# Performance work log

Hardware: AMD Instinct MI355X
Metric: run time of the kernel (lower is better)

The kernel has to match this reference:

```python
import jax, jax.numpy as jnp
import numpy as np

H = 256          # hidden_channels
NP, NJ, NC = 8192, 8192, 4096  # person / job_posting / company node counts
EA, EW, EP = 262144, 131072, 131072  # edge counts per relation


def _gcn(x_src, W, b, edge_index, num_src, num_dst):
    """Bipartite GCNConv: h = x_src @ W; out[dst] = sum_e norm_e * h[src_e] + b,
    norm = deg_out(src)^-1/2 * deg_in(dst)^-1/2 (symmetric GCN normalization)."""
    h = x_src @ W                                # [num_src, H]
    row, col = edge_index[0], edge_index[1]
    ones = jnp.ones(row.shape[0], dtype=h.dtype)
    deg_src = jax.ops.segment_sum(ones, row, num_segments=num_src)
    deg_dst = jax.ops.segment_sum(ones, col, num_segments=num_dst)
    dis_src = jnp.where(deg_src > 0, jax.lax.rsqrt(jnp.maximum(deg_src, 1e-12)), 0.0)
    dis_dst = jnp.where(deg_dst > 0, jax.lax.rsqrt(jnp.maximum(deg_dst, 1e-12)), 0.0)
    norm = dis_src[row] * dis_dst[col]           # [E]
    out = jax.ops.segment_sum(h[row] * norm[:, None], col, num_segments=num_dst)
    return out + b


def setup_inputs() -> dict:
    key = jax.random.key(0)
    ks = jax.random.split(key, 12)
    s = 1.0 / np.sqrt(H)
    return {
        "x_person":  jax.random.normal(ks[0], (NP, H), jnp.float32),
        "x_job":     jax.random.normal(ks[1], (NJ, H), jnp.float32),
        "x_company": jax.random.normal(ks[2], (NC, H), jnp.float32),
        "ei_applied": jax.random.randint(ks[3], (2, EA), 0, 8192, jnp.int64 if jax.config.read('jax_enable_x64') else jnp.int32),
        "ei_worked":  jax.random.randint(ks[4], (2, EW), 0, 4096, jnp.int64 if jax.config.read('jax_enable_x64') else jnp.int32),
        "ei_posted":  jax.random.randint(ks[5], (2, EP), 0, 4096, jnp.int64 if jax.config.read('jax_enable_x64') else jnp.int32),
        "W_aj": jax.random.normal(ks[6], (H, H), jnp.float32) * s,
        "b_aj": jnp.zeros((H,), jnp.float32),
        "W_wa": jax.random.normal(ks[7], (H, H), jnp.float32) * s,
        "b_wa": jnp.zeros((H,), jnp.float32),
        "W_pb": jax.random.normal(ks[8], (H, H), jnp.float32) * s,
        "b_pb": jnp.zeros((H,), jnp.float32),
    }


def reference(x_person, x_job, x_company, ei_applied, ei_worked, ei_posted,
              W_aj, b_aj, W_wa, b_wa, W_pb, b_pb):
    Np, Nj, Nc = x_person.shape[0], x_job.shape[0], x_company.shape[0]
    # HeteroConv with aggr='sum': each dst type sums messages over its edge types
    job_emb = _gcn(x_person, W_aj, b_aj, ei_applied, Np, Nj)
    comp_emb = (_gcn(x_person, W_wa, b_wa, ei_worked, Np, Nc)
                + _gcn(x_job, W_pb, b_pb, ei_posted, Nj, Nc))  # computed but unused downstream
    del comp_emb
    person_emb = x_person  # 'person' is never a dst type; features pass through
    scores = jax.nn.sigmoid(person_emb @ job_emb.T)  # [Np, Nj]
    return scores
```

## Files before the change

kernel.cpp:

```cpp
#include <hip/hip_runtime.h>
#include <hip/hip_bf16.h>

#define HCH 256
#define NPN 8192
#define NJN 8192
#define EAE 262144
#define CAP 96

typedef _Float16 f16x8 __attribute__((ext_vector_type(8)));
typedef _Float16 f16x4 __attribute__((ext_vector_type(4)));
typedef float f32x4 __attribute__((ext_vector_type(4)));

typedef __attribute__((address_space(1))) void glb_void;
typedef __attribute__((address_space(3))) void lds_void;

#define WS_CUR   0
#define WS_DEG   32768
#define WS_CSR2  65536
#define WS_XH    3211264
#define WS_ZH    7405568
#define WS_GH    11599872
#define WS_WHT   15794176

__global__ void k_init(int* __restrict__ cnt, const float* __restrict__ W,
                       _Float16* __restrict__ WhT, const float* __restrict__ x,
                       _Float16* __restrict__ Xh) {
    int bid = blockIdx.x, t = threadIdx.x;
    if (bid < 64) {
        cnt[bid * 256 + t] = 0;
    } else if (bid < 320) {
        int idx = (bid - 64) * 256 + t;
        int n = idx >> 8, k = idx & 255;
        WhT[idx] = (_Float16)W[k * HCH + n];
    } else {
        int i = ((bid - 320) * 256 + t) * 4;
        float4 v = *(const float4*)(x + i);
        f16x4 h;
        h[0] = (_Float16)v.x; h[1] = (_Float16)v.y;
        h[2] = (_Float16)v.z; h[3] = (_Float16)v.w;
        *(f16x4*)(Xh + i) = h;
    }
}

__global__ void k_edge(const int* __restrict__ row, const int* __restrict__ col,
                       int* __restrict__ deg_src, int* __restrict__ cur,
                       int* __restrict__ csr2) {
    int e = blockIdx.x * 256 + threadIdx.x;
    int r = row[e], c = col[e];
    atomicAdd(&deg_src[r], 1);
    int p = atomicAdd(&cur[c], 1);
    if (p < CAP) csr2[c * CAP + p] = r;
}

__global__ __launch_bounds__(64)
void k_agg(const _Float16* __restrict__ Xh, const int* __restrict__ csr2,
           const int* __restrict__ cur, const int* __restrict__ deg_src,
           _Float16* __restrict__ Zh) {
    int j = blockIdx.x;
    int t = threadIdx.x;
    int degt = cur[j];
    int deg = degt > CAP ? CAP : degt;

    __shared__ int   sidx[CAP];
    __shared__ float sw[CAP];
    for (int b = t; b < deg; b += 64) {
        int s = csr2[j * CAP + b];
        sidx[b] = s;
        sw[b] = rsqrtf((float)deg_src[s]);
    }
    __syncthreads();

    float a0 = 0.f, a1 = 0.f, a2 = 0.f, a3 = 0.f;
    const _Float16* xb = Xh + t * 4;
    int e = 0;
    for (; e + 4 <= deg; e += 4) {
        int s0 = sidx[e], s1 = sidx[e + 1], s2 = sidx[e + 2], s3 = sidx[e + 3];
        float w0 = sw[e], w1 = sw[e + 1], w2 = sw[e + 2], w3 = sw[e + 3];
        f16x4 v0 = *(const f16x4*)(xb + (size_t)s0 * HCH);
        f16x4 v1 = *(const f16x4*)(xb + (size_t)s1 * HCH);
        f16x4 v2 = *(const f16x4*)(xb + (size_t)s2 * HCH);
        f16x4 v3 = *(const f16x4*)(xb + (size_t)s3 * HCH);
        a0 += w0 * (float)v0[0] + w1 * (float)v1[0] + w2 * (float)v2[0] + w3 * (float)v3[0];
        a1 += w0 * (float)v0[1] + w1 * (float)v1[1] + w2 * (float)v2[1] + w3 * (float)v3[1];
        a2 += w0 * (float)v0[2] + w1 * (float)v1[2] + w2 * (float)v2[2] + w3 * (float)v3[2];
        a3 += w0 * (float)v0[3] + w1 * (float)v1[3] + w2 * (float)v2[3] + w3 * (float)v3[3];
    }
    for (; e < deg; e++) {
        int s0 = sidx[e];
        float w0 = sw[e];
        f16x4 v0 = *(const f16x4*)(xb + (size_t)s0 * HCH);
        a0 += w0 * (float)v0[0]; a1 += w0 * (float)v0[1];
        a2 += w0 * (float)v0[2]; a3 += w0 * (float)v0[3];
    }
    f16x4 out;
    if (degt > 0) {
        float dd = rsqrtf((float)degt);
        out[0] = (_Float16)(a0 * dd); out[1] = (_Float16)(a1 * dd);
        out[2] = (_Float16)(a2 * dd); out[3] = (_Float16)(a3 * dd);
    } else {
        out[0] = out[1] = out[2] = out[3] = (_Float16)0.f;
    }
    *(f16x4*)(Zh + (size_t)j * HCH + t * 4) = out;
}

template <int TM, int TN>
__global__ __launch_bounds__(256, 2)
void k_gemm(const _Float16* __restrict__ A, const _Float16* __restrict__ Bt,
            const float* __restrict__ bias, _Float16* __restrict__ Cout, int Ncols) {
    constexpr int WM = TM / 2, WN = TN / 2;
    constexpr int MR = WM / 16, NR = WN / 16;
    constexpr int CHA = TM * 8 / 256;
    constexpr int CHB = TN * 8 / 256;
    constexpr int BOFF = TM * 128;

    __shared__ _Float16 sm[2][(TM + TN) * 64];

    int tid = threadIdx.x;
    int wid = tid >> 6, lane = tid & 63;

    int brow = blockIdx.y * TM;
    int bcol = blockIdx.x * TN;
    int wrow = (wid >> 1) * WM;
    int wcol = (wid & 1) * WN;

    f32x4 acc[MR][NR] = {};

    int lr = lane & 15;
    int kq = lane >> 4;

    auto stage = [&](int t, int b) {
        int k0 = t * 64;
#pragma unroll
        for (int i = 0; i < CHA; i++) {
            int wc0 = i * 256 + wid * 64;
            int c = wc0 + lane;
            int r = c >> 3, cc = c & 7;
            const char* ga = (const char*)A +
                (size_t)(brow + r) * (HCH * 2) + (size_t)(k0 + cc * 8) * 2;
            __builtin_amdgcn_global_load_lds(
                (glb_void*)ga, (lds_void*)((char*)sm[b] + wc0 * 16), 16, 0, 0);
        }
#pragma unroll
        for (int i = 0; i < CHB; i++) {
            int wc0 = i * 256 + wid * 64;
            int c = wc0 + lane;
            int r = c >> 3, cc = c & 7;
            const char* gb = (const char*)Bt +
                (size_t)(bcol + r) * (HCH * 2) + (size_t)(k0 + cc * 8) * 2;
            __builtin_amdgcn_global_load_lds(
                (glb_void*)gb, (lds_void*)((char*)sm[b] + BOFF + wc0 * 16), 16, 0, 0);
        }
    };

    stage(0, 0);
    __syncthreads();

    constexpr int NT = HCH / 64;
#pragma unroll
    for (int t = 0; t < NT; t++) {
        int cur = t & 1;
        if (t + 1 < NT) stage(t + 1, cur ^ 1);
        const char* base = (const char*)sm[cur];
#pragma unroll
        for (int kk = 0; kk < 64; kk += 32) {
            f16x8 af[MR], bfr[NR];
            int kbyte = (kk + kq * 8) * 2;
#pragma unroll
            for (int m = 0; m < MR; m++) {
                int r = wrow + m * 16 + lr;
                af[m] = *(const f16x8*)(base + r * 128 + kbyte);
            }
#pragma unroll
            for (int n = 0; n < NR; n++) {
                int r = wcol + n * 16 + lr;
                bfr[n] = *(const f16x8*)(base + BOFF + r * 128 + kbyte);
            }
#pragma unroll
            for (int m = 0; m < MR; m++)
#pragma unroll
                for (int n = 0; n < NR; n++)
                    acc[m][n] = __builtin_amdgcn_mfma_f32_16x16x32_f16(
                        af[m], bfr[n], acc[m][n], 0, 0, 0);
        }
        __syncthreads();
    }

    int rq = lane >> 4;
#pragma unroll
    for (int m = 0; m < MR; m++) {
#pragma unroll
        for (int n = 0; n < NR; n++) {
#pragma unroll
            for (int j = 0; j < 4; j++) {
                int gr = brow + wrow + m * 16 + rq * 4 + j;
                int gc = bcol + wcol + n * 16 + lr;
                float v = acc[m][n][j] + bias[gc];
                Cout[(size_t)gr * Ncols + gc] = (_Float16)v;
            }
        }
    }
}

#define G2_NW 32
__global__ __launch_bounds__(512, 1)
void k_gemm2(const _Float16* __restrict__ A, const _Float16* __restrict__ Bt,
             float* __restrict__ C) {
    __shared__ _Float16 smA[128 * HCH];
    __shared__ _Float16 smB[2][64 * HCH];
    __shared__ float    smC[128 * 64];

    int tid = threadIdx.x;
    int wid = tid >> 6, lane = tid & 63;
    int lr = lane & 15, kq = lane >> 4;

    int id = blockIdx.x;
    int xcd = id & 7, slot = id >> 3;
    int cg = xcd >> 1;
    int strip = slot + (xcd & 1) * 32;
    int brow = strip * 128;
    int bcol0 = cg * (64 * G2_NW);

    int wrow = (wid >> 1) * 32;
    int wcol = (wid & 1) * 32;

#pragma unroll
    for (int i = 0; i < 8; i++) {
        int wc0 = i * 512 + wid * 64;
        int c = wc0 + lane;
        int r = c >> 5, q = c & 31;
        int j = q ^ (r & 7);
        const char* ga = (const char*)(A + (size_t)(brow + r) * HCH + j * 8);
        __builtin_amdgcn_global_load_lds(
            (glb_void*)ga, (lds_void*)((char*)smA + wc0 * 16), 16, 0, 0);
    }
    auto stageB = [&](int t, int b) {
#pragma unroll
        for (int i = 0; i < 4; i++) {
            int wc0 = i * 512 + wid * 64;
            int c = wc0 + lane;
            int r = c >> 5, q = c & 31;
            int j = q ^ (r & 7);
            const char* gb = (const char*)(Bt +
                (size_t)(bcol0 + t * 64 + r) * HCH + j * 8);
            __builtin_amdgcn_global_load_lds(
                (glb_void*)gb, (lds_void*)((char*)smB[b] + wc0 * 16), 16, 0, 0);
        }
    };
    stageB(0, 0);
    __syncthreads();

    const char* sA = (const char*)smA;
    f16x8 areg[2][8];
#pragma unroll
    for (int m = 0; m < 2; m++) {
#pragma unroll
        for (int ks = 0; ks < 8; ks++) {
            int r = wrow + m * 16 + lr;
            int sb = ks * 4 + kq;
            areg[m][ks] = *(const f16x8*)(sA + r * 512 + ((sb ^ (r & 7)) << 4));
        }
    }

    for (int t = 0; t < G2_NW; t++) {
        int cb = t & 1;
        if (t + 1 < G2_NW) stageB(t + 1, cb ^ 1);
        __builtin_amdgcn_sched_barrier(0);
        const char* sB = (const char*)smB[cb];
        f32x4 acc[2][2] = {};
        __builtin_amdgcn_s_setprio(1);
#pragma unroll
        for (int ks = 0; ks < 8; ks++) {
            f16x8 bf2[2];
            int sb = ks * 4 + kq;
#pragma unroll
            for (int n = 0; n < 2; n++) {
                int r = wcol + n * 16 + lr;
                bf2[n] = *(const f16x8*)(sB + r * 512 + ((sb ^ (r & 7)) << 4));
            }
#pragma unroll
            for (int m = 0; m < 2; m++)
#pragma unroll
                for (int n = 0; n < 2; n++)
                    acc[m][n] = __builtin_amdgcn_mfma_f32_16x16x32_f16(
                        bf2[n], areg[m][ks], acc[m][n], 0, 0, 0);
        }
        __builtin_amdgcn_s_setprio(0);

#pragma unroll
        for (int m = 0; m < 2; m++) {
#pragma unroll
            for (int n = 0; n < 2; n++) {
                int row = wrow + m * 16 + lr;
                int ch = ((wcol + n * 16) >> 2) + kq;
                int sc = ch ^ (row & 7);
                *(f32x4*)(smC + row * 64 + sc * 4) = acc[m][n];
            }
        }

        int bcol = bcol0 + t * 64;
        int ch = (wcol >> 2) + (lane & 7);
#pragma unroll
        for (int p = 0; p < 4; p++) {
            int row = wrow + p * 8 + (lane >> 3);
            int sc = ch ^ (row & 7);
            f32x4 v = *(const f32x4*)(smC + row * 64 + sc * 4);
            f32x4 o;
#pragma unroll
            for (int j = 0; j < 4; j++) {
                float e = __expf(-v[j]);
                o[j] = __builtin_amdgcn_rcpf(1.f + e);
            }
            __builtin_nontemporal_store(
                o, (f32x4*)(C + (size_t)(brow + row) * NJN + bcol + ch * 4));
        }

        if (t + 1 < G2_NW) {
            __builtin_amdgcn_sched_barrier(0);
            asm volatile("s_waitcnt vmcnt(4)" ::: "memory");
            __builtin_amdgcn_s_barrier();
            __builtin_amdgcn_sched_barrier(0);
        }
    }
}

extern "C" void kernel_launch(void* const* d_in, const int* in_sizes, int n_in,
                              void* d_out, int out_size, void* d_ws, size_t ws_size,
                              hipStream_t stream) {
    const float* x_person = (const float*)d_in[0];
    const int*   ei_app   = (const int*)d_in[3];
    const float* W_aj     = (const float*)d_in[6];
    const float* b_aj     = (const float*)d_in[7];

    const int* erow = ei_app;
    const int* ecol = ei_app + EAE;

    char* w = (char*)d_ws;
    int*      cur     = (int*)(w + WS_CUR);
    int*      deg_src = (int*)(w + WS_DEG);
    int*      csr2    = (int*)(w + WS_CSR2);
    _Float16* Xh      = (_Float16*)(w + WS_XH);
    _Float16* Zh      = (_Float16*)(w + WS_ZH);
    _Float16* Gh      = (_Float16*)(w + WS_GH);
    _Float16* WhT     = (_Float16*)(w + WS_WHT);

    k_init<<<2368, 256, 0, stream>>>(cur, W_aj, WhT, x_person, Xh);
    k_edge<<<EAE / 256, 256, 0, stream>>>(erow, ecol, deg_src, cur, csr2);
    k_agg<<<NJN, 64, 0, stream>>>(Xh, csr2, cur, deg_src, Zh);
    {
        dim3 grid(HCH / 128, NJN / 64);
        k_gemm<64, 128><<<grid, 256, 0, stream>>>(Zh, WhT, b_aj, Gh, HCH);
    }
    k_gemm2<<<256, 512, 0, stream>>>(Xh, Gh, (float*)d_out);
}
```

Before: 126.2 us.

## Fuse neighbor aggregation with the W projection GEMM into one kernel

Replaces the separate aggregation kernel and the small GEMM with one kernel. Each 512-thread block aggregates 32 job rows into swizzled LDS and then multiplies them by W, streaming W tiles through double-buffered LDS, before writing Gh. This removes the Zh round trip through global memory and one launch. In exchange there are only 256 blocks of 512 threads at one block per CU, so the gather phase may have less latency hiding than the old 8192 small blocks.

```diff
diff --git a/kernel.cpp b/kernel.cpp
--- a/kernel.cpp
+++ b/kernel.cpp
@@ -18,7 +18,6 @@
 #define WS_DEG   32768
 #define WS_CSR2  65536
 #define WS_XH    3211264
-#define WS_ZH    7405568
 #define WS_GH    11599872
 #define WS_WHT   15794176
 
@@ -52,151 +51,121 @@
     if (p < CAP) csr2[c * CAP + p] = r;
 }
 
-__global__ __launch_bounds__(64)
-void k_agg(const _Float16* __restrict__ Xh, const int* __restrict__ csr2,
-           const int* __restrict__ cur, const int* __restrict__ deg_src,
-           _Float16* __restrict__ Zh) {
-    int j = blockIdx.x;
-    int t = threadIdx.x;
-    int degt = cur[j];
-    int deg = degt > CAP ? CAP : degt;
-
-    __shared__ int   sidx[CAP];
-    __shared__ float sw[CAP];
-    for (int b = t; b < deg; b += 64) {
-        int s = csr2[j * CAP + b];
-        sidx[b] = s;
-        sw[b] = rsqrtf((float)deg_src[s]);
-    }
-    __syncthreads();
-
-    float a0 = 0.f, a1 = 0.f, a2 = 0.f, a3 = 0.f;
-    const _Float16* xb = Xh + t * 4;
-    int e = 0;
-    for (; e + 4 <= deg; e += 4) {
-        int s0 = sidx[e], s1 = sidx[e + 1], s2 = sidx[e + 2], s3 = sidx[e + 3];
-        float w0 = sw[e], w1 = sw[e + 1], w2 = sw[e + 2], w3 = sw[e + 3];
-        f16x4 v0 = *(const f16x4*)(xb + (size_t)s0 * HCH);
-        f16x4 v1 = *(const f16x4*)(xb + (size_t)s1 * HCH);
-        f16x4 v2 = *(const f16x4*)(xb + (size_t)s2 * HCH);
-        f16x4 v3 = *(const f16x4*)(xb + (size_t)s3 * HCH);
-        a0 += w0 * (float)v0[0] + w1 * (float)v1[0] + w2 * (float)v2[0] + w3 * (float)v3[0];
-        a1 += w0 * (float)v0[1] + w1 * (float)v1[1] + w2 * (float)v2[1] + w3 * (float)v3[1];
-        a2 += w0 * (float)v0[2] + w1 * (float)v1[2] + w2 * (float)v2[2] + w3 * (float)v3[2];
-        a3 += w0 * (float)v0[3] + w1 * (float)v1[3] + w2 * (float)v2[3] + w3 * (float)v3[3];
-    }
-    for (; e < deg; e++) {
-        int s0 = sidx[e];
-        float w0 = sw[e];
-        f16x4 v0 = *(const f16x4*)(xb + (size_t)s0 * HCH);
-        a0 += w0 * (float)v0[0]; a1 += w0 * (float)v0[1];
-        a2 += w0 * (float)v0[2]; a3 += w0 * (float)v0[3];
-    }
-    f16x4 out;
-    if (degt > 0) {
-        float dd = rsqrtf((float)degt);
-        out[0] = (_Float16)(a0 * dd); out[1] = (_Float16)(a1 * dd);
-        out[2] = (_Float16)(a2 * dd); out[3] = (_Float16)(a3 * dd);
-    } else {
-        out[0] = out[1] = out[2] = out[3] = (_Float16)0.f;
-    }
-    *(f16x4*)(Zh + (size_t)j * HCH + t * 4) = out;
-}
-
-template <int TM, int TN>
-__global__ __launch_bounds__(256, 2)
-void k_gemm(const _Float16* __restrict__ A, const _Float16* __restrict__ Bt,
-            const float* __restrict__ bias, _Float16* __restrict__ Cout, int Ncols) {
-    constexpr int WM = TM / 2, WN = TN / 2;
-    constexpr int MR = WM / 16, NR = WN / 16;
-    constexpr int CHA = TM * 8 / 256;
-    constexpr int CHB = TN * 8 / 256;
-    constexpr int BOFF = TM * 128;
-
-    __shared__ _Float16 sm[2][(TM + TN) * 64];
+__global__ __launch_bounds__(512, 1)
+void k_aggemm1(const _Float16* __restrict__ Xh, const int* __restrict__ csr2,
+               const int* __restrict__ cur, const int* __restrict__ deg_src,
+               const _Float16* __restrict__ WhT, const float* __restrict__ bias,
+               _Float16* __restrict__ Gh) {
+    __shared__ _Float16 smZ[32 * HCH];
+    __shared__ _Float16 smW[2][64 * HCH];
+    __shared__ int      sidxAll[8][96];
+    __shared__ float    swAll[8][96];
 
     int tid = threadIdx.x;
     int wid = tid >> 6, lane = tid & 63;
-
-    int brow = blockIdx.y * TM;
-    int bcol = blockIdx.x * TN;
-    int wrow = (wid >> 1) * WM;
-    int wcol = (wid & 1) * WN;
-
-    f32x4 acc[MR][NR] = {};
-
-    int lr = lane & 15;
-    int kq = lane >> 4;
-
-    auto stage = [&](int t, int b) {
-        int k0 = t * 64;
-#pragma unroll
-        for (int i = 0; i < CHA; i++) {
-            int wc0 = i * 256 + wid * 64;
+    int lr = lane & 15, kq = lane >> 4;
+    int brow = blockIdx.x * 32;
+
+    auto stageB = [&](int ct, int b) {
+#pragma unroll
+        for (int i = 0; i < 4; i++) {
+            int wc0 = i * 512 + wid * 64;
             int c = wc0 + lane;
-            int r = c >> 3, cc = c & 7;
-            const char* ga = (const char*)A +
-                (size_t)(brow + r) * (HCH * 2) + (size_t)(k0 + cc * 8) * 2;
+            int r = c >> 5, q = c & 31;
+            int j = q ^ (r & 7);
+            const char* gb = (const char*)(WhT +
+                (size_t)(ct * 64 + r) * HCH + j * 8);
             __builtin_amdgcn_global_load_lds(
-                (glb_void*)ga, (lds_void*)((char*)sm[b] + wc0 * 16), 16, 0, 0);
-        }
-#pragma unroll
-        for (int i = 0; i < CHB; i++) {
-            int wc0 = i * 256 + wid * 64;
-            int c = wc0 + lane;
-            int r = c >> 3, cc = c & 7;
-            const char* gb = (const char*)Bt +
-                (size_t)(bcol + r) * (HCH * 2) + (size_t)(k0 + cc * 8) * 2;
-            __builtin_amdgcn_global_load_lds(
-                (glb_void*)gb, (lds_void*)((char*)sm[b] + BOFF + wc0 * 16), 16, 0, 0);
+                (glb_void*)gb, (lds_void*)((char*)smW[b] + wc0 * 16), 16, 0, 0);
         }
     };
-
-    stage(0, 0);
+    stageB(0, 0);
+
+    int* sidx = sidxAll[wid];
+    float* sw = swAll[wid];
+#pragma unroll
+    for (int pass = 0; pass < 4; pass++) {
+        int jloc = pass * 8 + wid;
+        int j = brow + jloc;
+        int degt = cur[j];
+        int deg = degt > CAP ? CAP : degt;
+        for (int b = lane; b < deg; b += 64) {
+            int s = csr2[j * CAP + b];
+            sidx[b] = s;
+            sw[b] = rsqrtf((float)deg_src[s]);
+        }
+        float a0 = 0.f, a1 = 0.f, a2 = 0.f, a3 = 0.f;
+        const _Float16* xb = Xh + lane * 4;
+        int e = 0;
+        for (; e + 4 <= deg; e += 4) {
+            int s0 = sidx[e], s1 = sidx[e + 1], s2 = sidx[e + 2], s3 = sidx[e + 3];
+            float w0 = sw[e], w1 = sw[e + 1], w2 = sw[e + 2], w3 = sw[e + 3];
+            f16x4 v0 = *(const f16x4*)(xb + (size_t)s0 * HCH);
+            f16x4 v1 = *(const f16x4*)(xb + (size_t)s1 * HCH);
+            f16x4 v2 = *(const f16x4*)(xb + (size_t)s2 * HCH);
+            f16x4 v3 = *(const f16x4*)(xb + (size_t)s3 * HCH);
+            a0 += w0 * (float)v0[0] + w1 * (float)v1[0] + w2 * (float)v2[0] + w3 * (float)v3[0];
+            a1 += w0 * (float)v0[1] + w1 * (float)v1[1] + w2 * (float)v2[1] + w3 * (float)v3[1];
+            a2 += w0 * (float)v0[2] + w1 * (float)v1[2] + w2 * (float)v2[2] + w3 * (float)v3[2];
+            a3 += w0 * (float)v0[3] + w1 * (float)v1[3] + w2 * (float)v2[3] + w3 * (float)v3[3];
+        }
+        for (; e < deg; e++) {
+            int s0 = sidx[e];
+            float w0 = sw[e];
+            f16x4 v0 = *(const f16x4*)(xb + (size_t)s0 * HCH);
+            a0 += w0 * (float)v0[0]; a1 += w0 * (float)v0[1];
+            a2 += w0 * (float)v0[2]; a3 += w0 * (float)v0[3];
+        }
+        f16x4 out;
+        if (degt > 0) {
+            float dd = rsqrtf((float)degt);
+            out[0] = (_Float16)(a0 * dd); out[1] = (_Float16)(a1 * dd);
+            out[2] = (_Float16)(a2 * dd); out[3] = (_Float16)(a3 * dd);
+        } else {
+            out[0] = out[1] = out[2] = out[3] = (_Float16)0.f;
+        }
+        int byteoff = jloc * 512 + (((lane >> 1) ^ (jloc & 7)) << 4) + (lane & 1) * 8;
+        *(f16x4*)((char*)smZ + byteoff) = out;
+    }
     __syncthreads();
 
-    constexpr int NT = HCH / 64;
-#pragma unroll
-    for (int t = 0; t < NT; t++) {
-        int cur = t & 1;
-        if (t + 1 < NT) stage(t + 1, cur ^ 1);
-        const char* base = (const char*)sm[cur];
-#pragma unroll
-        for (int kk = 0; kk < 64; kk += 32) {
-            f16x8 af[MR], bfr[NR];
-            int kbyte = (kk + kq * 8) * 2;
-#pragma unroll
-            for (int m = 0; m < MR; m++) {
-                int r = wrow + m * 16 + lr;
-                af[m] = *(const f16x8*)(base + r * 128 + kbyte);
-            }
-#pragma unroll
-            for (int n = 0; n < NR; n++) {
-                int r = wcol + n * 16 + lr;
-                bfr[n] = *(const f16x8*)(base + BOFF + r * 128 + kbyte);
-            }
-#pragma unroll
-            for (int m = 0; m < MR; m++)
-#pragma unroll
-                for (int n = 0; n < NR; n++)
-                    acc[m][n] = __builtin_amdgcn_mfma_f32_16x16x32_f16(
-                        af[m], bfr[n], acc[m][n], 0, 0, 0);
-        }
-        __syncthreads();
-    }
-
-    int rq = lane >> 4;
-#pragma unroll
-    for (int m = 0; m < MR; m++) {
-#pragma unroll
-        for (int n = 0; n < NR; n++) {
-#pragma unroll
-            for (int j = 0; j < 4; j++) {
-                int gr = brow + wrow + m * 16 + rq * 4 + j;
-                int gc = bcol + wcol + n * 16 + lr;
-                float v = acc[m][n][j] + bias[gc];
-                Cout[(size_t)gr * Ncols + gc] = (_Float16)v;
-            }
+    int m = wid >> 2, n = wid & 3;
+    int arow = m * 16 + lr;
+
+    f16x8 areg[8];
+#pragma unroll
+    for (int ks = 0; ks < 8; ks++) {
+        int sb = ks * 4 + kq;
+        areg[ks] = *(const f16x8*)((const char*)smZ + arow * 512 +
+                                   ((sb ^ (arow & 7)) << 4));
+    }
+
+    for (int ct = 0; ct < 4; ct++) {
+        int cb = ct & 1;
+        if (ct + 1 < 4) stageB(ct + 1, cb ^ 1);
+        __builtin_amdgcn_sched_barrier(0);
+        const char* sB = (const char*)smW[cb];
+        f32x4 acc = {};
+#pragma unroll
+        for (int ks = 0; ks < 8; ks++) {
+            int sb = ks * 4 + kq;
+            int r = n * 16 + lr;
+            f16x8 bf = *(const f16x8*)(sB + r * 512 + ((sb ^ (r & 7)) << 4));
+            acc = __builtin_amdgcn_mfma_f32_16x16x32_f16(bf, areg[ks], acc, 0, 0, 0);
+        }
+        int gr = brow + m * 16 + lr;
+        int gc0 = ct * 64 + n * 16 + kq * 4;
+        float4 bv = *(const float4*)(bias + gc0);
+        f16x4 o;
+        o[0] = (_Float16)(acc[0] + bv.x); o[1] = (_Float16)(acc[1] + bv.y);
+        o[2] = (_Float16)(acc[2] + bv.z); o[3] = (_Float16)(acc[3] + bv.w);
+        *(f16x4*)(Gh + (size_t)gr * HCH + gc0) = o;
+
+        if (ct + 1 < 4) {
+            __builtin_amdgcn_sched_barrier(0);
+            asm volatile("s_waitcnt vmcnt(1)" ::: "memory");
+            __builtin_amdgcn_s_barrier();
+            __builtin_amdgcn_sched_barrier(0);
         }
     }
 }
@@ -215,10 +184,10 @@
 
     int id = blockIdx.x;
     int xcd = id & 7, slot = id >> 3;
-    int cg = xcd >> 1;
+    int cg2 = xcd >> 1;
     int strip = slot + (xcd & 1) * 32;
     int brow = strip * 128;
-    int bcol0 = cg * (64 * G2_NW);
+    int bcol0 = cg2 * (64 * G2_NW);
 
     int wrow = (wid >> 1) * 32;
     int wcol = (wid & 1) * 32;
@@ -339,16 +308,12 @@
     int*      deg_src = (int*)(w + WS_DEG);
     int*      csr2    = (int*)(w + WS_CSR2);
     _Float16* Xh      = (_Float16*)(w + WS_XH);
-    _Float16* Zh      = (_Float16*)(w + WS_ZH);
     _Float16* Gh      = (_Float16*)(w + WS_GH);
     _Float16* WhT     = (_Float16*)(w + WS_WHT);
 
     k_init<<<2368, 256, 0, stream>>>(cur, W_aj, WhT, x_person, Xh);
     k_edge<<<EAE / 256, 256, 0, stream>>>(erow, ecol, deg_src, cur, csr2);
-    k_agg<<<NJN, 64, 0, stream>>>(Xh, csr2, cur, deg_src, Zh);
-    {
-        dim3 grid(HCH / 128, NJN / 64);
-        k_gemm<64, 128><<<grid, 256, 0, stream>>>(Zh, WhT, b_aj, Gh, HCH);
-    }
+    k_aggemm1<<<NJN / 32, 512, 0, stream>>>(Xh, csr2, cur, deg_src, WhT,
+                                            b_aj, Gh);
     k_gemm2<<<256, 512, 0, stream>>>(Xh, Gh, (float*)d_out);
 }
```

After: 133.0 us. +5.3%, slower.

## Load B tiles directly from global into registers, dropping LDS double buffer

Applied to the files above, without the earlier changes.

The final sigmoid GEMM no longer stages B tiles through a double-buffered LDS array with async global-to-LDS loads and per-tile barriers. Each wave now reads its own B fragments straight from global memory (L2) into registers before its MFMAs. This removes the block-wide barriers and LDS traffic, and frees LDS. In exchange, B data shared by the four wave rows is fetched redundantly from cache, and load latency is no longer hidden by prefetch, so the MFMAs may stall on each tile's loads.

```diff
diff --git a/kernel.cpp b/kernel.cpp
--- a/kernel.cpp
+++ b/kernel.cpp
@@ -206,7 +206,6 @@
 void k_gemm2(const _Float16* __restrict__ A, const _Float16* __restrict__ Bt,
              float* __restrict__ C) {
     __shared__ _Float16 smA[128 * HCH];
-    __shared__ _Float16 smB[2][64 * HCH];
     __shared__ float    smC[128 * 64];
 
     int tid = threadIdx.x;
@@ -215,10 +214,10 @@
 
     int id = blockIdx.x;
     int xcd = id & 7, slot = id >> 3;
-    int cg = xcd >> 1;
+    int cg2 = xcd >> 1;
     int strip = slot + (xcd & 1) * 32;
     int brow = strip * 128;
-    int bcol0 = cg * (64 * G2_NW);
+    int bcol0 = cg2 * (64 * G2_NW);
 
     int wrow = (wid >> 1) * 32;
     int wcol = (wid & 1) * 32;
@@ -233,20 +232,6 @@
         __builtin_amdgcn_global_load_lds(
             (glb_void*)ga, (lds_void*)((char*)smA + wc0 * 16), 16, 0, 0);
     }
-    auto stageB = [&](int t, int b) {
-#pragma unroll
-        for (int i = 0; i < 4; i++) {
-            int wc0 = i * 512 + wid * 64;
-            int c = wc0 + lane;
-            int r = c >> 5, q = c & 31;
-            int j = q ^ (r & 7);
-            const char* gb = (const char*)(Bt +
-                (size_t)(bcol0 + t * 64 + r) * HCH + j * 8);
-            __builtin_amdgcn_global_load_lds(
-                (glb_void*)gb, (lds_void*)((char*)smB[b] + wc0 * 16), 16, 0, 0);
-        }
-    };
-    stageB(0, 0);
     __syncthreads();
 
     const char* sA = (const char*)smA;
@@ -262,28 +247,25 @@
     }
 
     for (int t = 0; t < G2_NW; t++) {
-        int cb = t & 1;
-        if (t + 1 < G2_NW) stageB(t + 1, cb ^ 1);
-        __builtin_amdgcn_sched_barrier(0);
-        const char* sB = (const char*)smB[cb];
+        int rowb = bcol0 + t * 64 + wcol;
+        f16x8 bf[2][8];
+#pragma unroll
+        for (int n = 0; n < 2; n++)
+#pragma unroll
+            for (int ks = 0; ks < 8; ks++)
+                bf[n][ks] = *(const f16x8*)(Bt +
+                    (size_t)(rowb + n * 16 + lr) * HCH + (ks * 4 + kq) * 8);
+
         f32x4 acc[2][2] = {};
         __builtin_amdgcn_s_setprio(1);
 #pragma unroll
-        for (int ks = 0; ks < 8; ks++) {
-            f16x8 bf2[2];
-            int sb = ks * 4 + kq;
-#pragma unroll
-            for (int n = 0; n < 2; n++) {
-                int r = wcol + n * 16 + lr;
-                bf2[n] = *(const f16x8*)(sB + r * 512 + ((sb ^ (r & 7)) << 4));
-            }
+        for (int ks = 0; ks < 8; ks++)
 #pragma unroll
             for (int m = 0; m < 2; m++)
 #pragma unroll
                 for (int n = 0; n < 2; n++)
                     acc[m][n] = __builtin_amdgcn_mfma_f32_16x16x32_f16(
-                        bf2[n], areg[m][ks], acc[m][n], 0, 0, 0);
-        }
+                        bf[n][ks], areg[m][ks], acc[m][n], 0, 0, 0);
         __builtin_amdgcn_s_setprio(0);
 
 #pragma unroll
@@ -312,13 +294,6 @@
             }
             __builtin_nontemporal_store(
                 o, (f32x4*)(C + (size_t)(brow + row) * NJN + bcol + ch * 4));
-        }
-
-        if (t + 1 < G2_NW) {
-            __builtin_amdgcn_sched_barrier(0);
-            asm volatile("s_waitcnt vmcnt(4)" ::: "memory");
-            __builtin_amdgcn_s_barrier();
-            __builtin_amdgcn_sched_barrier(0);
         }
     }
 }
```

Result: slower. 176.3 us (+39.6%).
